# Performance work log

Hardware: AMD Instinct MI355X
Metric: run time of the kernel (lower is better)

## Reference

```python
import jax, jax.numpy as jnp
import numpy as np

N_NODES = 50000


def _gin_aggregate(x, src, dst):
    # sum_{j in N(i)} x_j via scatter-add over edges; eps=0 so add self term
    msg = x[src]  # [E, d]
    return x + jax.ops.segment_sum(msg, dst, num_segments=N_NODES)


def _mlp(h, Wa, ba, Wb, bb):
    return jax.nn.relu(h @ Wa + ba) @ Wb + bb


def setup_inputs() -> dict:
    key = jax.random.key(0)
    ks = jax.random.split(key, 12)
    d_in, d_h, n_cls, n_edges = 128, 128, 40, 800000
    x = jax.random.normal(ks[0], (N_NODES, d_in), dtype=jnp.float32)
    edge_index = jax.random.randint(ks[1], (2, n_edges), 0, N_NODES, dtype=jnp.int64)
    s = lambda k, sh: jax.random.normal(k, sh, dtype=jnp.float32) / np.sqrt(sh[0])
    return {
        "x": x,
        "edge_index": edge_index,
        "W11": s(ks[2], (d_in, 2 * d_h)), "b11": jnp.zeros((2 * d_h,), jnp.float32),
        "W12": s(ks[3], (2 * d_h, d_h)), "b12": jnp.zeros((d_h,), jnp.float32),
        "W21": s(ks[4], (d_h, 2 * d_h)), "b21": jnp.zeros((2 * d_h,), jnp.float32),
        "W22": s(ks[5], (2 * d_h, d_h)), "b22": jnp.zeros((d_h,), jnp.float32),
        "Wfc": s(ks[6], (d_h, n_cls)), "bfc": jnp.zeros((n_cls,), jnp.float32),
    }


def reference(x, edge_index, W11, b11, W12, b12, W21, b21, W22, b22, Wfc, bfc):
    src, dst = edge_index[0], edge_index[1]
    # GINConv 1: aggregate then MLP, followed by ReLU
    h = _mlp(_gin_aggregate(x, src, dst), W11, b11, W12, b12)
    h = jax.nn.relu(h)
    # GINConv 2
    h = _mlp(_gin_aggregate(h, src, dst), W21, b21, W22, b22)
    h = jax.nn.relu(h)
    # final classifier
    return h @ Wfc + bfc
```

## Files before the change

### kernel.cpp

```cpp
#include <hip/hip_runtime.h>

#define N_NODES 50000
#define N_EDGES 800000
#define NBUCK   392
#define EPB     2048
#define NSB     391
#define CAPB    2560

typedef __attribute__((ext_vector_type(8))) short short8;
typedef __attribute__((ext_vector_type(4))) float floatx4;

__device__ __forceinline__ float ubits(unsigned int b) {
    union { unsigned int i; float f; } v;
    v.i = b;
    return v.f;
}
__device__ __forceinline__ unsigned short f2b(float f) {
    union { float f; unsigned int i; } v;
    v.f = f;
    unsigned int r = v.i + 0x7FFFu + ((v.i >> 16) & 1u);
    return (unsigned short)(r >> 16);
}

__global__ __launch_bounds__(256) void hist_conv(
    const int* __restrict__ dstv, const float* __restrict__ x,
    int* __restrict__ cnt, unsigned short* __restrict__ xb) {
    const int bid = blockIdx.x;
    const int tid = threadIdx.x;
    if (bid < NSB) {
        __shared__ int hist[NBUCK];
        const int k = bid;
        const int e0 = k * EPB;
        for (int i = tid; i < NBUCK; i += 256) hist[i] = 0;
        __syncthreads();
#pragma unroll
        for (int j = 0; j < EPB / 256; ++j) {
            int e = e0 + j * 256 + tid;
            if (e < N_EDGES) atomicAdd(&hist[dstv[e] >> 7], 1);
        }
        __syncthreads();
        for (int i = tid; i < NBUCK; i += 256) cnt[i * NSB + k] = hist[i];
    } else {
        int i = (bid - NSB) * 256 + tid;
        const float4 a = *reinterpret_cast<const float4*>(x + (size_t)i * 8);
        const float4 b = *reinterpret_cast<const float4*>(x + (size_t)i * 8 + 4);
        ushort4 u0, u1;
        u0.x = f2b(a.x); u0.y = f2b(a.y); u0.z = f2b(a.z); u0.w = f2b(a.w);
        u1.x = f2b(b.x); u1.y = f2b(b.y); u1.z = f2b(b.z); u1.w = f2b(b.w);
        *reinterpret_cast<ushort4*>(xb + (size_t)i * 8) = u0;
        *reinterpret_cast<ushort4*>(xb + (size_t)i * 8 + 4) = u1;
    }
}

__global__ __launch_bounds__(256) void scan_conv(
    const int* __restrict__ cnt, int* __restrict__ sbase,
    const float* __restrict__ W11, const float* __restrict__ W12,
    const float* __restrict__ W21, const float* __restrict__ W22,
    const float* __restrict__ Wfc,
    unsigned short* __restrict__ Wt11, unsigned short* __restrict__ Wt12,
    unsigned short* __restrict__ Wt21, unsigned short* __restrict__ Wt22,
    unsigned short* __restrict__ Wfct) {
    const int bid = blockIdx.x;
    const int tid = threadIdx.x;
    if (bid < NBUCK) {
        __shared__ int ps[256];
        __shared__ int sc[512];
        const int b = bid;
        sc[tid] = (tid < NSB) ? cnt[b * NSB + tid] : 0;
        sc[tid + 256] = (tid + 256 < NSB) ? cnt[b * NSB + tid + 256] : 0;
        __syncthreads();
        const int c0 = sc[2 * tid], c1 = sc[2 * tid + 1];
        ps[tid] = c0 + c1;
        __syncthreads();
        for (int off = 1; off < 256; off <<= 1) {
            int u = (tid >= off) ? ps[tid - off] : 0;
            __syncthreads();
            ps[tid] += u;
            __syncthreads();
        }
        if (tid < 196) {
            const int off0 = ps[tid] - (c0 + c1);
            sbase[b * 392 + 2 * tid] = off0;
            sbase[b * 392 + 2 * tid + 1] = off0 + c0;
        }
    } else if (bid < NBUCK + 512) {
        int wb = bid - NBUCK;
        int which = wb >> 7;
        int idx = (wb & 127) * 256 + tid;
        const float* W = (which == 0) ? W11 : (which == 1) ? W12 : (which == 2) ? W21 : W22;
        unsigned short* Wt = (which == 0) ? Wt11 : (which == 1) ? Wt12 : (which == 2) ? Wt21 : Wt22;
        int K = (which & 1) ? 256 : 128;
        int N = (which & 1) ? 128 : 256;
        int k = idx / N, n = idx - k * N;
        Wt[n * K + k] = f2b(W[idx]);
    } else {
        int idx = (bid - NBUCK - 512) * 256 + tid;
        int n = idx >> 7, k = idx & 127;
        Wfct[idx] = (n < 40) ? f2b(Wfc[k * 40 + n]) : (unsigned short)0;
    }
}

__global__ __launch_bounds__(256) void place_compact(
    const int* __restrict__ srcv, const int* __restrict__ dstv,
    const int* __restrict__ sbase, int* __restrict__ bufc) {
    __shared__ int cur[NBUCK];
    const int k = blockIdx.x;
    const int tid = threadIdx.x;
    for (int i = tid; i < NBUCK; i += 256) cur[i] = sbase[i * 392 + k];
    __syncthreads();
    const int e0 = k * EPB;
#pragma unroll
    for (int j = 0; j < EPB / 256; ++j) {
        int e = e0 + j * 256 + tid;
        if (e < N_EDGES) {
            int d = dstv[e];
            int b = d >> 7;
            int pos = atomicAdd(&cur[b], 1);
            bufc[b * CAPB + pos] = srcv[e] | ((d & 127) << 16);
        }
    }
}

__global__ __launch_bounds__(256) void finish_buckets(
    const int* __restrict__ sbase, const int* __restrict__ bufc,
    int* __restrict__ e_src, int* __restrict__ row_ptr) {
    __shared__ int nc[128];
    __shared__ int ps[128];
    const int b = blockIdx.x;
    const int tid = threadIdx.x;
    const int S = sbase[b * 392 + 391];
    const int gb = b * CAPB;
    if (tid < 128) nc[tid] = 0;
    __syncthreads();
    for (int t = tid; t < S; t += 256)
        atomicAdd(&nc[(bufc[gb + t] >> 16) & 127], 1);
    __syncthreads();
    if (tid < 128) ps[tid] = nc[tid];
    __syncthreads();
    for (int off = 1; off < 128; off <<= 1) {
        int u = (tid >= off && tid < 128) ? ps[tid - off] : 0;
        __syncthreads();
        if (tid < 128) ps[tid] += u;
        __syncthreads();
    }
    if (tid < 128) {
        const int excl = ps[tid] - nc[tid];
        row_ptr[b * 129 + tid] = gb + excl;
        nc[tid] = gb + excl;
    }
    if (tid == 0) row_ptr[b * 129 + 128] = gb + S;
    __syncthreads();
    for (int t = tid; t < S; t += 256) {
        int p = bufc[gb + t];
        int pos = atomicAdd(&nc[(p >> 16) & 127], 1);
        e_src[pos] = p & 0xFFFF;
    }
}

__global__ __launch_bounds__(256) void agg_bf16q(const unsigned short* __restrict__ X,
                                                 const int* __restrict__ row_ptr,
                                                 const int* __restrict__ e_src,
                                                 unsigned short* __restrict__ agg) {
    const int node = (blockIdx.x * 256 + threadIdx.x) >> 6;
    const int lane = threadIdx.x & 63;
    const int qw = lane >> 4, ql = lane & 15;
    const size_t off = (size_t)ql * 8;

    const int rp = node + (node >> 7);
    const int beg = row_ptr[rp], end = row_ptr[rp + 1];
    float acc[8];
#pragma unroll
    for (int k = 0; k < 8; ++k) acc[k] = 0.f;

    if (qw == 0) {
        uint4 u = *reinterpret_cast<const uint4*>(X + (size_t)node * 128 + off);
        const unsigned int* up = (const unsigned int*)&u;
#pragma unroll
        for (int k = 0; k < 4; ++k) {
            acc[2 * k]     += ubits(up[k] << 16);
            acc[2 * k + 1] += ubits(up[k] & 0xFFFF0000u);
        }
    }

    int e = beg + qw;
    for (; e + 12 < end; e += 16) {
        const int s0 = e_src[e], s1 = e_src[e + 4], s2 = e_src[e + 8], s3 = e_src[e + 12];
        uint4 u0 = *reinterpret_cast<const uint4*>(X + (size_t)s0 * 128 + off);
        uint4 u1 = *reinterpret_cast<const uint4*>(X + (size_t)s1 * 128 + off);
        uint4 u2 = *reinterpret_cast<const uint4*>(X + (size_t)s2 * 128 + off);
        uint4 u3 = *reinterpret_cast<const uint4*>(X + (size_t)s3 * 128 + off);
        const unsigned int* p0 = (const unsigned int*)&u0;
        const unsigned int* p1 = (const unsigned int*)&u1;
        const unsigned int* p2 = (const unsigned int*)&u2;
        const unsigned int* p3 = (const unsigned int*)&u3;
#pragma unroll
        for (int k = 0; k < 4; ++k) {
            acc[2 * k]     += ubits(p0[k] << 16) + ubits(p1[k] << 16)
                            + ubits(p2[k] << 16) + ubits(p3[k] << 16);
            acc[2 * k + 1] += ubits(p0[k] & 0xFFFF0000u) + ubits(p1[k] & 0xFFFF0000u)
                            + ubits(p2[k] & 0xFFFF0000u) + ubits(p3[k] & 0xFFFF0000u);
        }
    }
    for (; e + 4 < end; e += 8) {
        const int s0 = e_src[e], s1 = e_src[e + 4];
        uint4 u0 = *reinterpret_cast<const uint4*>(X + (size_t)s0 * 128 + off);
        uint4 u1 = *reinterpret_cast<const uint4*>(X + (size_t)s1 * 128 + off);
        const unsigned int* p0 = (const unsigned int*)&u0;
        const unsigned int* p1 = (const unsigned int*)&u1;
#pragma unroll
        for (int k = 0; k < 4; ++k) {
            acc[2 * k]     += ubits(p0[k] << 16) + ubits(p1[k] << 16);
            acc[2 * k + 1] += ubits(p0[k] & 0xFFFF0000u) + ubits(p1[k] & 0xFFFF0000u);
        }
    }
    if (e < end) {
        const int s = e_src[e];
        uint4 u = *reinterpret_cast<const uint4*>(X + (size_t)s * 128 + off);
        const unsigned int* p = (const unsigned int*)&u;
#pragma unroll
        for (int k = 0; k < 4; ++k) {
            acc[2 * k]     += ubits(p[k] << 16);
            acc[2 * k + 1] += ubits(p[k] & 0xFFFF0000u);
        }
    }

#pragma unroll
    for (int k = 0; k < 8; ++k) acc[k] += __shfl_xor(acc[k], 32);
#pragma unroll
    for (int k = 0; k < 8; ++k) acc[k] += __shfl_xor(acc[k], 16);

    if (qw == 0) {
        ushort4 o0, o1;
        o0.x = f2b(acc[0]); o0.y = f2b(acc[1]); o0.z = f2b(acc[2]); o0.w = f2b(acc[3]);
        o1.x = f2b(acc[4]); o1.y = f2b(acc[5]); o1.z = f2b(acc[6]); o1.w = f2b(acc[7]);
        unsigned short* p = agg + (size_t)node * 128 + off;
        *reinterpret_cast<ushort4*>(p) = o0;
        *reinterpret_cast<ushort4*>(p + 4) = o1;
    }
}

template <bool FUSE>
__global__ __launch_bounds__(256, FUSE ? 2 : 3) void mlp_fused(
    const unsigned short* __restrict__ X, const unsigned short* __restrict__ Wt1,
    const float* __restrict__ b1, const unsigned short* __restrict__ Wt2,
    const float* __restrict__ b2, unsigned short* __restrict__ Y,
    const unsigned short* __restrict__ Wfct, const float* __restrict__ bfc,
    float* __restrict__ out, int M) {
    __shared__ __align__(16) char smem[FUSE ? 69632 : 52224];
    unsigned short* A   = (unsigned short*)smem;
    unsigned short* B2q = (unsigned short*)smem;
    unsigned short* B1h = (unsigned short*)(smem + 17408);
    unsigned short* T   = (unsigned short*)(smem + 17408);
    unsigned short* Hf  = (unsigned short*)(smem + 52224);

    const int tid = threadIdx.x;
    const int m0 = blockIdx.x * 64;
    const int lane = tid & 63, w = tid >> 6;
    const int qm = lane & 15, quad = lane >> 4;

#pragma unroll
    for (int j = 0; j < 4; ++j) {
        int i = j * 256 + tid;
        int r = i >> 4, c8 = (i & 15) << 3;
        uint4 v = {0, 0, 0, 0};
        if (m0 + r < M) v = *reinterpret_cast<const uint4*>(X + (size_t)(m0 + r) * 128 + c8);
        *reinterpret_cast<uint4*>(&A[r * 136 + c8]) = v;
    }

    floatx4 acc1[2][4][2];
#pragma unroll
    for (int c = 0; c < 2; ++c)
#pragma unroll
        for (int mt = 0; mt < 4; ++mt)
#pragma unroll
            for (int nt = 0; nt < 2; ++nt) acc1[c][mt][nt] = {0.f, 0.f, 0.f, 0.f};

    for (int c = 0; c < 2; ++c) {
#pragma unroll
        for (int j = 0; j < 8; ++j) {
            int i = j * 256 + tid;
            int r = i >> 4, c8 = (i & 15) << 3;
            *reinterpret_cast<uint4*>(&B1h[r * 136 + c8]) =
                *reinterpret_cast<const uint4*>(Wt1 + (size_t)(c * 128 + r) * 128 + c8);
        }
        __syncthreads();
#pragma unroll
        for (int ks = 0; ks < 4; ++ks) {
            const int kb = ks * 32 + quad * 8;
            short8 a[4], b[2];
#pragma unroll
            for (int mt = 0; mt < 4; ++mt)
                a[mt] = *reinterpret_cast<const short8*>(&A[(mt * 16 + qm) * 136 + kb]);
#pragma unroll
            for (int nt = 0; nt < 2; ++nt)
                b[nt] = *reinterpret_cast<const short8*>(&B1h[(w * 32 + nt * 16 + qm) * 136 + kb]);
#pragma unroll
            for (int mt = 0; mt < 4; ++mt)
#pragma unroll
                for (int nt = 0; nt < 2; ++nt)
                    acc1[c][mt][nt] = __builtin_amdgcn_mfma_f32_16x16x32_bf16(
                        a[mt], b[nt], acc1[c][mt][nt], 0, 0, 0);
        }
        __syncthreads();
    }

#pragma unroll
    for (int c = 0; c < 2; ++c) {
#pragma unroll
        for (int nt = 0; nt < 2; ++nt) {
            const int jcol = c * 128 + w * 32 + nt * 16 + qm;
            const float bj = b1[jcol];
#pragma unroll
            for (int mt = 0; mt < 4; ++mt)
#pragma unroll
                for (int r = 0; r < 4; ++r)
                    T[(mt * 16 + quad * 4 + r) * 264 + jcol] =
                        f2b(fmaxf(acc1[c][mt][nt][r] + bj, 0.f));
        }
    }

    for (int c2 = 0; c2 < 4; ++c2) {
#pragma unroll
        for (int j = 0; j < 4; ++j) {
            int i = j * 256 + tid;
            int r = i >> 5, c8 = (i & 31) << 3;
            *reinterpret_cast<uint4*>(&B2q[r * 264 + c8]) =
                *reinterpret_cast<const uint4*>(Wt2 + (size_t)(c2 * 32 + r) * 256 + c8);
        }
        __syncthreads();

        floatx4 acc2[2];
        acc2[0] = {0.f, 0.f, 0.f, 0.f};
        acc2[1] = {0.f, 0.f, 0.f, 0.f};
#pragma unroll
        for (int ks = 0; ks < 8; ++ks) {
            const int kb = ks * 32 + quad * 8;
            short8 t0 = *reinterpret_cast<const short8*>(&T[((w & 1) * 32 + qm) * 264 + kb]);
            short8 t1 = *reinterpret_cast<const short8*>(&T[((w & 1) * 32 + 16 + qm) * 264 + kb]);
            short8 bb = *reinterpret_cast<const short8*>(&B2q[((w >> 1) * 16 + qm) * 264 + kb]);
            acc2[0] = __builtin_amdgcn_mfma_f32_16x16x32_bf16(t0, bb, acc2[0], 0, 0, 0);
            acc2[1] = __builtin_amdgcn_mfma_f32_16x16x32_bf16(t1, bb, acc2[1], 0, 0, 0);
        }

        const int ncol = c2 * 32 + (w >> 1) * 16 + qm;
        const float bj = b2[ncol];
        if (!FUSE) {
#pragma unroll
            for (int mt2 = 0; mt2 < 2; ++mt2)
#pragma unroll
                for (int r = 0; r < 4; ++r) {
                    int row = m0 + (w & 1) * 32 + mt2 * 16 + quad * 4 + r;
                    if (row < M)
                        Y[(size_t)row * 128 + ncol] = f2b(fmaxf(acc2[mt2][r] + bj, 0.f));
                }
        } else {
#pragma unroll
            for (int mt2 = 0; mt2 < 2; ++mt2)
#pragma unroll
                for (int r = 0; r < 4; ++r)
                    Hf[((w & 1) * 32 + mt2 * 16 + quad * 4 + r) * 136 + ncol] =
                        f2b(fmaxf(acc2[mt2][r] + bj, 0.f));
        }
        __syncthreads();
    }

    if (FUSE) {
        floatx4 cacc[3];
#pragma unroll
        for (int nt = 0; nt < 3; ++nt) cacc[nt] = {0.f, 0.f, 0.f, 0.f};
#pragma unroll
        for (int c2 = 0; c2 < 4; ++c2) {
            short8 hf = *reinterpret_cast<const short8*>(
                &Hf[(w * 16 + qm) * 136 + c2 * 32 + quad * 8]);
#pragma unroll
            for (int nt = 0; nt < 3; ++nt) {
                short8 bf = *reinterpret_cast<const short8*>(
                    Wfct + (nt * 16 + qm) * 128 + c2 * 32 + quad * 8);
                cacc[nt] = __builtin_amdgcn_mfma_f32_16x16x32_bf16(hf, bf, cacc[nt], 0, 0, 0);
            }
        }
#pragma unroll
        for (int nt = 0; nt < 3; ++nt) {
            int col = nt * 16 + qm;
            if (col < 40) {
                const float bj = bfc[col];
#pragma unroll
                for (int r = 0; r < 4; ++r) {
                    int row = m0 + w * 16 + quad * 4 + r;
                    if (row < M) out[(size_t)row * 40 + col] = cacc[nt][r] + bj;
                }
            }
        }
    }
}

extern "C" void kernel_launch(void* const* d_in, const int* in_sizes, int n_in,
                              void* d_out, int out_size, void* d_ws, size_t ws_size,
                              hipStream_t stream) {
    const float* x   = (const float*)d_in[0];
    const int*   ei  = (const int*)d_in[1];
    const float* W11 = (const float*)d_in[2];
    const float* b11 = (const float*)d_in[3];
    const float* W12 = (const float*)d_in[4];
    const float* b12 = (const float*)d_in[5];
    const float* W21 = (const float*)d_in[6];
    const float* b21 = (const float*)d_in[7];
    const float* W22 = (const float*)d_in[8];
    const float* b22 = (const float*)d_in[9];
    const float* Wfc = (const float*)d_in[10];
    const float* bfc = (const float*)d_in[11];
    float* out = (float*)d_out;

    const int* srcv = ei;
    const int* dstv = ei + N_EDGES;

    unsigned short* agg  = (unsigned short*)d_ws;
    unsigned short* h    = agg + (size_t)N_NODES * 128;
    unsigned short* xb   = h   + (size_t)N_NODES * 128;
    unsigned short* Wt11 = xb  + (size_t)N_NODES * 128;
    unsigned short* Wt12 = Wt11 + 256 * 128;
    unsigned short* Wt21 = Wt12 + 256 * 128;
    unsigned short* Wt22 = Wt21 + 256 * 128;
    unsigned short* Wfct = Wt22 + 256 * 128;
    int* cnt     = (int*)(Wfct + 48 * 128);
    int* sbase   = cnt + 153664;
    int* row_ptr = sbase + 153664;
    int* e_src   = row_ptr + 50688;
    int* bufc    = e_src + (size_t)NBUCK * CAPB;

    hist_conv<<<NSB + 3125, 256, 0, stream>>>(dstv, x, cnt, xb);

    scan_conv<<<NBUCK + 536, 256, 0, stream>>>(
        cnt, sbase, W11, W12, W21, W22, Wfc,
        Wt11, Wt12, Wt21, Wt22, Wfct);

    place_compact<<<NSB, 256, 0, stream>>>(srcv, dstv, sbase, bufc);

    finish_buckets<<<NBUCK, 256, 0, stream>>>(sbase, bufc, e_src, row_ptr);

    const int agg_blocks = N_NODES * 64 / 256;
    const int mlp_blocks = (N_NODES + 63) / 64;

    agg_bf16q<<<agg_blocks, 256, 0, stream>>>(xb, row_ptr, e_src, agg);
    mlp_fused<false><<<mlp_blocks, 256, 0, stream>>>(
        agg, Wt11, b11, Wt12, b12, h, nullptr, nullptr, nullptr, N_NODES);
    agg_bf16q<<<agg_blocks, 256, 0, stream>>>(h, row_ptr, e_src, agg);
    mlp_fused<true><<<mlp_blocks, 256, 0, stream>>>(
        agg, Wt21, b21, Wt22, b22, nullptr, Wfct, bfc, out, N_NODES);
}
```

Baseline: 232.6 us.

## Prepack MLP weights in MFMA fragment order and load them directly into registers

Weight preprocessing now writes the MLP weights in a per-lane MFMA fragment layout, so each thread loads its B operands with coalesced 16-byte global reads into registers. Staging the weights through LDS and the associated __syncthreads barriers are removed from the MLP kernel. The aim is to cut LDS traffic and barrier stalls in the GEMM stages. In exchange, register pressure rises (16 plus 32 short8 weight fragments per thread), the non-fused variant drops to 2 blocks per SM in its launch bounds, and every block re-reads the weights from global memory or L2.

```diff
diff --git a/kernel.cpp b/kernel.cpp
--- a/kernel.cpp
+++ b/kernel.cpp
@@ -20,6 +20,29 @@
     v.f = f;
     unsigned int r = v.i + 0x7FFFu + ((v.i >> 16) & 1u);
     return (unsigned short)(r >> 16);
+}
+
+__device__ __forceinline__ void pack_s1(const float* __restrict__ W,
+                                        unsigned short* __restrict__ Wp,
+                                        int blk, int tid) {
+    int p = blk * 256 + tid;
+    int j = p & 7, t2 = (p >> 3) & 255, v = p >> 11;
+    int w = t2 >> 6, lane = t2 & 63, quad = lane >> 4, qm = lane & 15;
+    int c = v >> 3, ks = (v >> 1) & 3, nt = v & 1;
+    int k = ks * 32 + quad * 8 + j;
+    int n = c * 128 + w * 32 + nt * 16 + qm;
+    Wp[p] = f2b(W[k * 256 + n]);
+}
+__device__ __forceinline__ void pack_s2(const float* __restrict__ W,
+                                        unsigned short* __restrict__ Wp,
+                                        int blk, int tid) {
+    int p = blk * 256 + tid;
+    int j = p & 7, t2 = (p >> 3) & 255, v2 = p >> 11;
+    int w = t2 >> 6, lane = t2 & 63, quad = lane >> 4, qm = lane & 15;
+    int c2 = v2 >> 3, ks = v2 & 7;
+    int k = ks * 32 + quad * 8 + j;
+    int n = c2 * 32 + (w >> 1) * 16 + qm;
+    Wp[p] = f2b(W[k * 128 + n]);
 }
 
 __global__ __launch_bounds__(256) void hist_conv(
@@ -57,8 +80,8 @@
     const float* __restrict__ W11, const float* __restrict__ W12,
     const float* __restrict__ W21, const float* __restrict__ W22,
     const float* __restrict__ Wfc,
-    unsigned short* __restrict__ Wt11, unsigned short* __restrict__ Wt12,
-    unsigned short* __restrict__ Wt21, unsigned short* __restrict__ Wt22,
+    unsigned short* __restrict__ Wp11, unsigned short* __restrict__ Wp12,
+    unsigned short* __restrict__ Wp21, unsigned short* __restrict__ Wp22,
     unsigned short* __restrict__ Wfct) {
     const int bid = blockIdx.x;
     const int tid = threadIdx.x;
@@ -83,18 +106,16 @@
             sbase[b * 392 + 2 * tid] = off0;
             sbase[b * 392 + 2 * tid + 1] = off0 + c0;
         }
+    } else if (bid < NBUCK + 128) {
+        pack_s1(W11, Wp11, bid - NBUCK, tid);
+    } else if (bid < NBUCK + 384) {
+        pack_s2(W12, Wp12, bid - NBUCK - 128, tid);
     } else if (bid < NBUCK + 512) {
-        int wb = bid - NBUCK;
-        int which = wb >> 7;
-        int idx = (wb & 127) * 256 + tid;
-        const float* W = (which == 0) ? W11 : (which == 1) ? W12 : (which == 2) ? W21 : W22;
-        unsigned short* Wt = (which == 0) ? Wt11 : (which == 1) ? Wt12 : (which == 2) ? Wt21 : Wt22;
-        int K = (which & 1) ? 256 : 128;
-        int N = (which & 1) ? 128 : 256;
-        int k = idx / N, n = idx - k * N;
-        Wt[n * K + k] = f2b(W[idx]);
+        pack_s1(W21, Wp21, bid - NBUCK - 384, tid);
+    } else if (bid < NBUCK + 768) {
+        pack_s2(W22, Wp22, bid - NBUCK - 512, tid);
     } else {
-        int idx = (bid - NBUCK - 512) * 256 + tid;
+        int idx = (bid - NBUCK - 768) * 256 + tid;
         int n = idx >> 7, k = idx & 127;
         Wfct[idx] = (n < 40) ? f2b(Wfc[k * 40 + n]) : (unsigned short)0;
     }
@@ -240,23 +261,26 @@
 }
 
 template <bool FUSE>
-__global__ __launch_bounds__(256, FUSE ? 2 : 3) void mlp_fused(
-    const unsigned short* __restrict__ X, const unsigned short* __restrict__ Wt1,
-    const float* __restrict__ b1, const unsigned short* __restrict__ Wt2,
+__global__ __launch_bounds__(256, 2) void mlp_fused(
+    const unsigned short* __restrict__ X, const unsigned short* __restrict__ Wp1,
+    const float* __restrict__ b1, const unsigned short* __restrict__ Wp2,
     const float* __restrict__ b2, unsigned short* __restrict__ Y,
     const unsigned short* __restrict__ Wfct, const float* __restrict__ bfc,
     float* __restrict__ out, int M) {
-    __shared__ __align__(16) char smem[FUSE ? 69632 : 52224];
-    unsigned short* A   = (unsigned short*)smem;
-    unsigned short* B2q = (unsigned short*)smem;
-    unsigned short* B1h = (unsigned short*)(smem + 17408);
-    unsigned short* T   = (unsigned short*)(smem + 17408);
-    unsigned short* Hf  = (unsigned short*)(smem + 52224);
+    __shared__ __align__(16) char smem[FUSE ? 68608 : 51200];
+    unsigned short* A  = (unsigned short*)smem;
+    unsigned short* T  = (unsigned short*)(smem + 17408);
+    unsigned short* Hf = (unsigned short*)(smem + 51200);
 
     const int tid = threadIdx.x;
     const int m0 = blockIdx.x * 64;
     const int lane = tid & 63, w = tid >> 6;
     const int qm = lane & 15, quad = lane >> 4;
+
+    short8 wb1[16];
+#pragma unroll
+    for (int v = 0; v < 16; ++v)
+        wb1[v] = *reinterpret_cast<const short8*>(Wp1 + ((v * 256 + tid) << 3));
 
 #pragma unroll
     for (int j = 0; j < 4; ++j) {
@@ -266,46 +290,29 @@
         if (m0 + r < M) v = *reinterpret_cast<const uint4*>(X + (size_t)(m0 + r) * 128 + c8);
         *reinterpret_cast<uint4*>(&A[r * 136 + c8]) = v;
     }
-
-    floatx4 acc1[2][4][2];
-#pragma unroll
-    for (int c = 0; c < 2; ++c)
+    __syncthreads();
+
+#pragma unroll
+    for (int c = 0; c < 2; ++c) {
+        floatx4 acc1[4][2];
 #pragma unroll
         for (int mt = 0; mt < 4; ++mt)
 #pragma unroll
-            for (int nt = 0; nt < 2; ++nt) acc1[c][mt][nt] = {0.f, 0.f, 0.f, 0.f};
-
-    for (int c = 0; c < 2; ++c) {
-#pragma unroll
-        for (int j = 0; j < 8; ++j) {
-            int i = j * 256 + tid;
-            int r = i >> 4, c8 = (i & 15) << 3;
-            *reinterpret_cast<uint4*>(&B1h[r * 136 + c8]) =
-                *reinterpret_cast<const uint4*>(Wt1 + (size_t)(c * 128 + r) * 128 + c8);
-        }
-        __syncthreads();
+            for (int nt = 0; nt < 2; ++nt) acc1[mt][nt] = {0.f, 0.f, 0.f, 0.f};
 #pragma unroll
         for (int ks = 0; ks < 4; ++ks) {
             const int kb = ks * 32 + quad * 8;
-            short8 a[4], b[2];
+            short8 a[4];
 #pragma unroll
             for (int mt = 0; mt < 4; ++mt)
                 a[mt] = *reinterpret_cast<const short8*>(&A[(mt * 16 + qm) * 136 + kb]);
 #pragma unroll
-            for (int nt = 0; nt < 2; ++nt)
-                b[nt] = *reinterpret_cast<const short8*>(&B1h[(w * 32 + nt * 16 + qm) * 136 + kb]);
-#pragma unroll
             for (int mt = 0; mt < 4; ++mt)
 #pragma unroll
                 for (int nt = 0; nt < 2; ++nt)
-                    acc1[c][mt][nt] = __builtin_amdgcn_mfma_f32_16x16x32_bf16(
-                        a[mt], b[nt], acc1[c][mt][nt], 0, 0, 0);
-        }
-        __syncthreads();
-    }
-
-#pragma unroll
-    for (int c = 0; c < 2; ++c) {
+                    acc1[mt][nt] = __builtin_amdgcn_mfma_f32_16x16x32_bf16(
+                        a[mt], wb1[c * 8 + ks * 2 + nt], acc1[mt][nt], 0, 0, 0);
+        }
 #pragma unroll
         for (int nt = 0; nt < 2; ++nt) {
             const int jcol = c * 128 + w * 32 + nt * 16 + qm;
@@ -315,20 +322,18 @@
 #pragma unroll
                 for (int r = 0; r < 4; ++r)
                     T[(mt * 16 + quad * 4 + r) * 264 + jcol] =
-                        f2b(fmaxf(acc1[c][mt][nt][r] + bj, 0.f));
-        }
-    }
-
+                        f2b(fmaxf(acc1[mt][nt][r] + bj, 0.f));
+        }
+    }
+
+    short8 wb2[32];
+#pragma unroll
+    for (int v = 0; v < 32; ++v)
+        wb2[v] = *reinterpret_cast<const short8*>(Wp2 + ((v * 256 + tid) << 3));
+    __syncthreads();
+
+#pragma unroll
     for (int c2 = 0; c2 < 4; ++c2) {
-#pragma unroll
-        for (int j = 0; j < 4; ++j) {
-            int i = j * 256 + tid;
-            int r = i >> 5, c8 = (i & 31) << 3;
-            *reinterpret_cast<uint4*>(&B2q[r * 264 + c8]) =
-                *reinterpret_cast<const uint4*>(Wt2 + (size_t)(c2 * 32 + r) * 256 + c8);
-        }
-        __syncthreads();
-
         floatx4 acc2[2];
         acc2[0] = {0.f, 0.f, 0.f, 0.f};
         acc2[1] = {0.f, 0.f, 0.f, 0.f};
@@ -337,9 +342,8 @@
             const int kb = ks * 32 + quad * 8;
             short8 t0 = *reinterpret_cast<const short8*>(&T[((w & 1) * 32 + qm) * 264 + kb]);
             short8 t1 = *reinterpret_cast<const short8*>(&T[((w & 1) * 32 + 16 + qm) * 264 + kb]);
-            short8 bb = *reinterpret_cast<const short8*>(&B2q[((w >> 1) * 16 + qm) * 264 + kb]);
-            acc2[0] = __builtin_amdgcn_mfma_f32_16x16x32_bf16(t0, bb, acc2[0], 0, 0, 0);
-            acc2[1] = __builtin_amdgcn_mfma_f32_16x16x32_bf16(t1, bb, acc2[1], 0, 0, 0);
+            acc2[0] = __builtin_amdgcn_mfma_f32_16x16x32_bf16(t0, wb2[c2 * 8 + ks], acc2[0], 0, 0, 0);
+            acc2[1] = __builtin_amdgcn_mfma_f32_16x16x32_bf16(t1, wb2[c2 * 8 + ks], acc2[1], 0, 0, 0);
         }
 
         const int ncol = c2 * 32 + (w >> 1) * 16 + qm;
@@ -361,10 +365,10 @@
                     Hf[((w & 1) * 32 + mt2 * 16 + quad * 4 + r) * 136 + ncol] =
                         f2b(fmaxf(acc2[mt2][r] + bj, 0.f));
         }
-        __syncthreads();
     }
 
     if (FUSE) {
+        __syncthreads();
         floatx4 cacc[3];
 #pragma unroll
         for (int nt = 0; nt < 3; ++nt) cacc[nt] = {0.f, 0.f, 0.f, 0.f};
@@ -417,11 +421,11 @@
     unsigned short* agg  = (unsigned short*)d_ws;
     unsigned short* h    = agg + (size_t)N_NODES * 128;
     unsigned short* xb   = h   + (size_t)N_NODES * 128;
-    unsigned short* Wt11 = xb  + (size_t)N_NODES * 128;
-    unsigned short* Wt12 = Wt11 + 256 * 128;
-    unsigned short* Wt21 = Wt12 + 256 * 128;
-    unsigned short* Wt22 = Wt21 + 256 * 128;
-    unsigned short* Wfct = Wt22 + 256 * 128;
+    unsigned short* Wp11 = xb  + (size_t)N_NODES * 128;
+    unsigned short* Wp12 = Wp11 + 32768;
+    unsigned short* Wp21 = Wp12 + 65536;
+    unsigned short* Wp22 = Wp21 + 32768;
+    unsigned short* Wfct = Wp22 + 65536;
     int* cnt     = (int*)(Wfct + 48 * 128);
     int* sbase   = cnt + 153664;
     int* row_ptr = sbase + 153664;
@@ -430,9 +434,9 @@
 
     hist_conv<<<NSB + 3125, 256, 0, stream>>>(dstv, x, cnt, xb);
 
-    scan_conv<<<NBUCK + 536, 256, 0, stream>>>(
+    scan_conv<<<NBUCK + 792, 256, 0, stream>>>(
         cnt, sbase, W11, W12, W21, W22, Wfc,
-        Wt11, Wt12, Wt21, Wt22, Wfct);
+        Wp11, Wp12, Wp21, Wp22, Wfct);
 
     place_compact<<<NSB, 256, 0, stream>>>(srcv, dstv, sbase, bufc);
 
@@ -443,8 +447,8 @@
 
     agg_bf16q<<<agg_blocks, 256, 0, stream>>>(xb, row_ptr, e_src, agg);
     mlp_fused<false><<<mlp_blocks, 256, 0, stream>>>(
-        agg, Wt11, b11, Wt12, b12, h, nullptr, nullptr, nullptr, N_NODES);
+        agg, Wp11, b11, Wp12, b12, h, nullptr, nullptr, nullptr, N_NODES);
     agg_bf16q<<<agg_blocks, 256, 0, stream>>>(h, row_ptr, e_src, agg);
     mlp_fused<true><<<mlp_blocks, 256, 0, stream>>>(
-        agg, Wt21, b21, Wt22, b22, nullptr, Wfct, bfc, out, N_NODES);
-}
+        agg, Wp21, b21, Wp22, b22, nullptr, Wfct, bfc, out, N_NODES);
+}
```

Result: faster. 226.1 us (-2.8%).
